# Optimization experiments

Measured on AMD Instinct MI355X. Metric: run time of the kernel, lower is better.

The kernel has to match this reference:

```python
import jax, jax.numpy as jnp
import numpy as np

EPS_R2 = 1e-12
EPS_POS = 1e-08
EPS_SUM = 1e-12


def _gaussian_psf(k, sigma):
    ax = np.arange(-k // 2 + 1.0, k // 2 + 1.0)
    xx, yy = np.meshgrid(ax, ax)
    g = np.exp(-(xx ** 2 + yy ** 2) / (2.0 * sigma ** 2))
    g = g / g.sum()
    return jnp.asarray(g.astype(np.float32))[None, None]  # (1,1,k,k)


def setup_inputs() -> dict:
    key = jax.random.key(0)
    k1, k2, k3 = jax.random.split(key, 3)
    B, C, H, W = 16, 1, 1024, 1024
    src = jax.random.normal(k1, (B, C, H, W), dtype=jnp.float32)
    raw_psf = _gaussian_psf(21, 3.0) + 0.001 * jax.random.normal(k2, (1, 1, 21, 21), dtype=jnp.float32)
    sub = 0.1 * jax.random.normal(k3, (2,), dtype=jnp.float32)
    return {
        "src": src,
        "raw_psf": raw_psf,
        "x0": jnp.float32(0.0),
        "y0": jnp.float32(0.0),
        "raw_b": jnp.float32(0.08),
        "raw_rc": jnp.float32(0.01),
        "raw_subpix": sub,
    }


def _bilinear_sample(src, gx, gy):
    # src: (B,C,H,W); gx, gy: (B,Hg,Wg) normalized coords in [-1,1],
    # align_corners=True, zeros padding (matches F.grid_sample).
    B, C, H, W = src.shape
    ix = (gx + 1.0) * 0.5 * (W - 1)
    iy = (gy + 1.0) * 0.5 * (H - 1)
    ix0 = jnp.floor(ix)
    iy0 = jnp.floor(iy)
    wx1 = ix - ix0
    wy1 = iy - iy0
    ix0i = ix0.astype(jnp.int32)
    iy0i = iy0.astype(jnp.int32)
    ix1i = ix0i + 1
    iy1i = iy0i + 1
    bidx = jnp.arange(B)[:, None, None]

    def corner(yi, xi, w):
        valid = (yi >= 0) & (yi < H) & (xi >= 0) & (xi < W)
        yc = jnp.clip(yi, 0, H - 1)
        xc = jnp.clip(xi, 0, W - 1)
        v = src[bidx, :, yc, xc]  # (B,Hg,Wg,C)
        return v * (w * valid)[..., None]

    out = (corner(iy0i, ix0i, (1.0 - wy1) * (1.0 - wx1))
           + corner(iy0i, ix1i, (1.0 - wy1) * wx1)
           + corner(iy1i, ix0i, wy1 * (1.0 - wx1))
           + corner(iy1i, ix1i, wy1 * wx1))
    return jnp.transpose(out, (0, 3, 1, 2))  # (B,C,Hg,Wg)


def reference(src, raw_psf, x0, y0, raw_b, raw_rc, raw_subpix):
    B, C, H, W = src.shape
    k = raw_psf.shape[-1]
    b = jax.nn.softplus(raw_b) + EPS_POS
    rc = jax.nn.softplus(raw_rc) + EPS_POS
    sub = 0.25 * jnp.tanh(raw_subpix)

    xs = jnp.linspace(-1.0, 1.0, W)
    ys = jnp.linspace(-1.0, 1.0, H)
    # torch.meshgrid(ys, xs, indexing='xy') semantics: shape (W, H),
    # yv[i,j] = ys[j], xv[i,j] = xs[i] (note: transposed vs usual HxW).
    yv, xv = jnp.meshgrid(ys, xs, indexing='xy')

    dx = xv - x0
    dy = yv - y0
    denom = jnp.sqrt(dx * dx + dy * dy + EPS_R2 + rc * rc)
    ax = b * dx / denom
    ay = b * dy / denom

    gx = jnp.broadcast_to(xv - ax + sub[0], (B, W, H))
    gy = jnp.broadcast_to(yv - ay + sub[1], (B, W, H))

    y_warp = _bilinear_sample(src, gx, gy)  # (B,C,W,H)

    psf = jnp.maximum(raw_psf, 0.0)
    psf = psf / jnp.maximum(psf.sum(axis=(2, 3), keepdims=True), EPS_SUM)
    pad = k // 2
    y_conv = jax.lax.conv_general_dilated(
        y_warp, psf, window_strides=(1, 1),
        padding=((pad, pad), (pad, pad)),
        dimension_numbers=("NCHW", "OIHW", "NCHW"))
    return y_conv
```

## Files before the change

### kernel.cpp

```cpp
#include <hip/hip_runtime.h>
#include <math.h>

#define WW 1024
#define HH 1024
#define TI 64
#define TJ 128
#define HALO_J 148
#define VALID_I 84
#define FILL_I 96
#define PITCH_T 104
#define AOFF 448
#define AOFF2 21952
#define YOFF 43520
#define NEED_WS (174080u + 33554432u)

typedef short short8 __attribute__((ext_vector_type(8)));
typedef float float16 __attribute__((ext_vector_type(16)));

__device__ __forceinline__ unsigned short f2bf(float f) {
    union { float f; unsigned int u; } c; c.f = f;
    unsigned int u = c.u;
    return (unsigned short)((u + 0x7FFFu + ((u >> 16) & 1u)) >> 16);
}

__device__ __forceinline__ float warp_sample(const float* __restrict__ sb, int I, int J,
                                             float bpar, float rc2, float sub0, float sub1,
                                             float x0, float y0) {
    const float SSTEP = 2.0f / 1023.0f;
    float yv = fmaf((float)J, SSTEP, -1.0f);
    float xv = fmaf((float)I, SSTEP, -1.0f);
    float dx = xv - x0;
    float dy = yv - y0;
    float s = bpar * __builtin_amdgcn_rsqf(dx * dx + dy * dy + rc2);
    float gx = xv - dx * s + sub0;
    float gy = yv - dy * s + sub1;
    float ix = (gx + 1.0f) * (0.5f * 1023.0f);
    float iy = (gy + 1.0f) * (0.5f * 1023.0f);
    float fx = floorf(ix), fy = floorf(iy);
    float wx1 = ix - fx, wy1 = iy - fy;
    float wx0 = 1.f - wx1, wy0 = 1.f - wy1;
    int xi0 = (int)fx, yi0 = (int)fy;
    int xi1 = xi0 + 1, yi1 = yi0 + 1;
    int xc0 = min(max(xi0, 0), WW - 1);
    int xc1 = min(max(xi1, 0), WW - 1);
    int yc0 = min(max(yi0, 0), HH - 1);
    int yc1 = min(max(yi1, 0), HH - 1);
    bool vx0 = (unsigned)xi0 < WW, vx1 = (unsigned)xi1 < WW;
    bool vy0 = (unsigned)yi0 < HH, vy1 = (unsigned)yi1 < HH;
    float w00 = (vx0 && vy0) ? wy0 * wx0 : 0.f;
    float w01 = (vx1 && vy0) ? wy0 * wx1 : 0.f;
    float w10 = (vx0 && vy1) ? wy1 * wx0 : 0.f;
    float w11 = (vx1 && vy1) ? wy1 * wx1 : 0.f;
    float v00 = sb[yc0 * WW + xc0];
    float v01 = sb[yc0 * WW + xc1];
    float v10 = sb[yc1 * WW + xc0];
    float v11 = sb[yc1 * WW + xc1];
    return v00 * w00 + v01 * w01 + v10 * w10 + v11 * w11;
}

__global__ void prep_kernel(const float* __restrict__ raw_psf,
                            const float* __restrict__ x0p, const float* __restrict__ y0p,
                            const float* __restrict__ raw_b, const float* __restrict__ raw_rc,
                            const float* __restrict__ raw_sub,
                            float* __restrict__ ws) {
    __shared__ float red[512];
    __shared__ float psn[441];
    int t = threadIdx.x;
    float v = 0.f;
    if (t < 441) v = fmaxf(raw_psf[t], 0.f);
    red[t] = v;
    __syncthreads();
    for (int s = 256; s > 0; s >>= 1) {
        if (t < s) red[t] += red[t + s];
        __syncthreads();
    }
    float sum = fmaxf(red[0], 1e-12f);
    if (t < 441) { float pn = v / sum; ws[t] = pn; psn[t] = pn; }
    if (t == 0) {
        float b  = log1pf(expf(raw_b[0]))  + 1e-8f;
        float rc = log1pf(expf(raw_rc[0])) + 1e-8f;
        ws[441] = b;
        ws[442] = 1e-12f + rc * rc;
        ws[443] = 0.25f * tanhf(raw_sub[0]);
        ws[444] = 0.25f * tanhf(raw_sub[1]);
        ws[445] = x0p[0];
        ws[446] = y0p[0];
    }
    __syncthreads();

    short* A  = (short*)(ws + AOFF);
    short* A2 = (short*)(ws + AOFF2);
    for (int g = t; g < 21 * 256; g += 512) {
        int vv = g >> 8;
        int r  = g & 255;
        int d  = r >> 6;
        int l  = r & 63;
        int m  = l & 31;
        int k0 = (l >> 5) << 3;
        short8 o8, o8b;
#pragma unroll
        for (int q = 0; q < 8; ++q) {
            int u = 16 * d + k0 + q - m;
            unsigned short pv = 0, pv2 = 0;
            if ((unsigned)u <= 20u) pv = f2bf(psn[u * 21 + vv]);
            int u2 = u - 6;
            if ((unsigned)u2 <= 20u) pv2 = f2bf(psn[u2 * 21 + vv]);
            o8[q]  = (short)pv;
            o8b[q] = (short)pv2;
        }
        *(short8*)&A[(size_t)g * 8]  = o8;
        *(short8*)&A2[(size_t)g * 8] = o8b;
    }
}

__global__ __launch_bounds__(256, 4) void warp_kernel(
        const float* __restrict__ src, const float* __restrict__ pp,
        unsigned short* __restrict__ yw) {
    const float bpar = pp[441], rc2 = pp[442];
    const float sub0 = pp[443], sub1 = pp[444];
    const float x0 = pp[445], y0 = pp[446];
    const int base = blockIdx.x * 8192;
    const int tid = threadIdx.x;
#pragma unroll 4
    for (int it = 0; it < 32; ++it) {
        int n = base + it * 256 + tid;
        int b0 = n >> 20;
        int J = (n >> 10) & 1023;
        int I = n & 1023;
        const float* sb = src + ((size_t)b0 << 20);
        float val = warp_sample(sb, I, J, bpar, rc2, sub0, sub1, x0, y0);
        yw[n] = f2bf(val);
    }
}

__global__ __launch_bounds__(256, 4) void conv_kernel(
        const unsigned short* __restrict__ yw, const float* __restrict__ pp,
        float* __restrict__ out) {
    __shared__ unsigned short ThT[HALO_J * PITCH_T];

    const int tid = threadIdx.x;
    const int j0 = blockIdx.x * TJ;
    const int i0 = blockIdx.y * TI;
    const int b0 = blockIdx.z;

    const unsigned short* wb = yw + ((size_t)b0 << 20);

    for (int p = tid; p < HALO_J * 12; p += 256) {
        int hc = (int)((unsigned)p / 12u);
        int c  = p - hc * 12;
        int J  = j0 - 10 + hc;
        int xs = i0 - 16 + c * 8;
        short8 d8 = {0, 0, 0, 0, 0, 0, 0, 0};
        if ((unsigned)J < HH && (unsigned)xs < WW)
            d8 = *(const short8*)&wb[J * WW + xs];
        *(short8*)&ThT[hc * PITCH_T + c * 8] = d8;
    }
    __syncthreads();

    const int lane = tid & 63;
    const int wv = tid >> 6;
    const int nrow = lane & 31;
    const int khalf = lane >> 5;

    float16 acc[2];
#pragma unroll
    for (int m = 0; m < 2; ++m)
#pragma unroll
        for (int q = 0; q < 16; ++q) acc[m][q] = 0.f;

    const short8* Aall = (const short8*)(pp + AOFF2);

#pragma unroll 1
    for (int v = 0; v < 21; ++v) {
        short8 Af[4];
#pragma unroll
        for (int d = 0; d < 4; ++d)
            Af[d] = Aall[(v * 4 + d) * 64 + lane];

        const unsigned short* bp = &ThT[(32 * wv + nrow + v) * PITCH_T + khalf * 8];
        short8 Bf[6];
#pragma unroll
        for (int c = 0; c < 6; ++c)
            Bf[c] = *(const short8*)&bp[16 * c];

#pragma unroll
        for (int mq = 0; mq < 2; ++mq) {
#pragma unroll
            for (int d = 0; d < 4; ++d)
                acc[mq] = __builtin_amdgcn_mfma_f32_32x32x16_bf16(
                    Af[d], Bf[2 * mq + d], acc[mq], 0, 0, 0);
        }
    }

    float* ob = out + (size_t)b0 * (WW * (size_t)HH);
    const int gj = j0 + 32 * wv + nrow;
#pragma unroll
    for (int mq = 0; mq < 2; ++mq) {
#pragma unroll
        for (int reg = 0; reg < 16; ++reg) {
            int row = (reg & 3) + 8 * (reg >> 2) + 4 * khalf;
            int gi = i0 + 32 * mq + row;
            ob[(size_t)gi * HH + gj] = acc[mq][reg];
        }
    }
}

__global__ __launch_bounds__(256, 4) void fused_kernel(
        const float* __restrict__ src, const float* __restrict__ pp,
        float* __restrict__ out) {
    __shared__ unsigned short ThT[HALO_J * PITCH_T];

    const int tid = threadIdx.x;
    const int j0 = blockIdx.x * TJ;
    const int i0 = blockIdx.y * TI;
    const int b0 = blockIdx.z;

    const float bpar = pp[441], rc2 = pp[442];
    const float sub0 = pp[443], sub1 = pp[444];
    const float x0 = pp[445], y0 = pp[446];

    const float* sb = src + (size_t)b0 * (HH * (size_t)WW);

    const int NELEM = HALO_J * FILL_I;
#pragma unroll 1
    for (int base = 0; base < NELEM; base += 1024) {
        float vals[4];
        int offs[4];
#pragma unroll
        for (int e = 0; e < 4; ++e) {
            int n = base + (e << 8) + tid;
            float val = 0.f;
            int off = -1;
            if (n < NELEM) {
                int hc = (int)((unsigned)n / 96u);
                int hr = n - hc * 96;
                off = hc * PITCH_T + hr;
                int J = j0 - 10 + hc;
                int I = i0 - 10 + hr;
                if (hr < VALID_I && (unsigned)J < HH && (unsigned)I < WW)
                    val = warp_sample(sb, I, J, bpar, rc2, sub0, sub1, x0, y0);
            }
            vals[e] = val;
            offs[e] = off;
        }
#pragma unroll
        for (int e = 0; e < 4; ++e) {
            if (offs[e] >= 0) ThT[offs[e]] = f2bf(vals[e]);
        }
    }
    __syncthreads();

    const int lane = tid & 63;
    const int wv = tid >> 6;
    const int nrow = lane & 31;
    const int khalf = lane >> 5;

    float16 acc[2];
#pragma unroll
    for (int m = 0; m < 2; ++m)
#pragma unroll
        for (int q = 0; q < 16; ++q) acc[m][q] = 0.f;

    const short8* Aall = (const short8*)(pp + AOFF);

#pragma unroll 1
    for (int v = 0; v < 21; ++v) {
        short8 Af[4];
#pragma unroll
        for (int d = 0; d < 4; ++d)
            Af[d] = Aall[(v * 4 + d) * 64 + lane];

        const unsigned short* bp = &ThT[(32 * wv + nrow + v) * PITCH_T + khalf * 8];
        short8 Bf[6];
#pragma unroll
        for (int c = 0; c < 6; ++c)
            Bf[c] = *(const short8*)&bp[16 * c];

#pragma unroll
        for (int mq = 0; mq < 2; ++mq) {
#pragma unroll
            for (int d = 0; d < 4; ++d)
                acc[mq] = __builtin_amdgcn_mfma_f32_32x32x16_bf16(
                    Af[d], Bf[2 * mq + d], acc[mq], 0, 0, 0);
        }
    }

    float* ob = out + (size_t)b0 * (WW * (size_t)HH);
    const int gj = j0 + 32 * wv + nrow;
#pragma unroll
    for (int mq = 0; mq < 2; ++mq) {
#pragma unroll
        for (int reg = 0; reg < 16; ++reg) {
            int row = (reg & 3) + 8 * (reg >> 2) + 4 * khalf;
            int gi = i0 + 32 * mq + row;
            ob[(size_t)gi * HH + gj] = acc[mq][reg];
        }
    }
}

extern "C" void kernel_launch(void* const* d_in, const int* in_sizes, int n_in,
                              void* d_out, int out_size, void* d_ws, size_t ws_size,
                              hipStream_t stream) {
    const float* src     = (const float*)d_in[0];
    const float* raw_psf = (const float*)d_in[1];
    const float* x0      = (const float*)d_in[2];
    const float* y0      = (const float*)d_in[3];
    const float* raw_b   = (const float*)d_in[4];
    const float* raw_rc  = (const float*)d_in[5];
    const float* raw_sub = (const float*)d_in[6];
    float* ws = (float*)d_ws;

    prep_kernel<<<1, 512, 0, stream>>>(raw_psf, x0, y0, raw_b, raw_rc, raw_sub, ws);

    dim3 grid(HH / TJ, WW / TI, 16);
    if (ws_size >= (size_t)NEED_WS) {
        unsigned short* yw = (unsigned short*)(ws + YOFF);
        warp_kernel<<<2048, 256, 0, stream>>>(src, ws, yw);
        conv_kernel<<<grid, 256, 0, stream>>>(yw, ws, (float*)d_out);
    } else {
        fused_kernel<<<grid, 256, 0, stream>>>(src, ws, (float*)d_out);
    }
}
```

Before: 216.9 us.

## Add in-bounds bilinear fast path in warp kernel and prefetch conv weights

Restructures the warp kernel so each block handles eight rows of one image and hoists per-row terms. It computes coordinates with a fast reciprocal square root and, when every lane of a wavefront is in bounds, does a plain 4-tap bilinear load without bounds checks; otherwise it falls back to the original sampler. The conv kernel now software-prefetches the next iteration's PSF fragments from global memory, hiding load latency behind the MFMAs. Risks are small numerical differences from rsq, and the prefetch reads one fragment past the last tap (v=21), which may step outside the weight array.

```diff
diff --git a/kernel.cpp b/kernel.cpp
--- a/kernel.cpp
+++ b/kernel.cpp
@@ -119,17 +119,68 @@
     const float bpar = pp[441], rc2 = pp[442];
     const float sub0 = pp[443], sub1 = pp[444];
     const float x0 = pp[445], y0 = pp[446];
-    const int base = blockIdx.x * 8192;
+    const float SSTEP = 2.0f / 1023.0f;
+
     const int tid = threadIdx.x;
-#pragma unroll 4
-    for (int it = 0; it < 32; ++it) {
-        int n = base + it * 256 + tid;
-        int b0 = n >> 20;
-        int J = (n >> 10) & 1023;
-        int I = n & 1023;
-        const float* sb = src + ((size_t)b0 << 20);
-        float val = warp_sample(sb, I, J, bpar, rc2, sub0, sub1, x0, y0);
-        yw[n] = f2bf(val);
+    const int nb  = blockIdx.x;
+    const int b0  = nb >> 7;
+    const int J0  = (nb & 127) << 3;
+    const float* sb = src + ((size_t)b0 << 20);
+    unsigned short* yb = yw + ((size_t)b0 << 20) + ((size_t)J0 << 10);
+
+#pragma unroll 1
+    for (int jr = 0; jr < 8; ++jr) {
+        int J = J0 + jr;
+        float yv = fmaf((float)J, SSTEP, -1.0f);
+        float dy = yv - y0;
+        float dyt = fmaf(dy, dy, rc2);
+        unsigned short* yrow = yb + (jr << 10);
+
+        float ixa[4], iya[4];
+        bool bad = false;
+#pragma unroll
+        for (int q = 0; q < 4; ++q) {
+            int I = (q << 8) + tid;
+            float xv = fmaf((float)I, SSTEP, -1.0f);
+            float dx = xv - x0;
+            float s  = bpar * __builtin_amdgcn_rsqf(fmaf(dx, dx, dyt));
+            float gx = xv - dx * s + sub0;
+            float gy = yv - dy * s + sub1;
+            ixa[q] = (gx + 1.0f) * (0.5f * 1023.0f);
+            iya[q] = (gy + 1.0f) * (0.5f * 1023.0f);
+            bad |= !(ixa[q] >= 0.f && ixa[q] < 1023.f &&
+                     iya[q] >= 0.f && iya[q] < 1023.f);
+        }
+        if (!__any(bad)) {
+            float v00[4], v01[4], v10[4], v11[4], fxs[4], fys[4];
+#pragma unroll
+            for (int q = 0; q < 4; ++q) {
+                float fx = floorf(ixa[q]), fy = floorf(iya[q]);
+                fxs[q] = fx; fys[q] = fy;
+                const float* p = sb + (((int)fy) << 10) + (int)fx;
+                v00[q] = p[0];
+                v01[q] = p[1];
+                v10[q] = p[WW];
+                v11[q] = p[WW + 1];
+            }
+#pragma unroll
+            for (int q = 0; q < 4; ++q) {
+                float wx1 = ixa[q] - fxs[q];
+                float wy1 = iya[q] - fys[q];
+                float wx0 = 1.f - wx1;
+                float r0 = fmaf(wx1, v01[q], wx0 * v00[q]);
+                float r1 = fmaf(wx1, v11[q], wx0 * v10[q]);
+                float val = fmaf(wy1, r1, (1.f - wy1) * r0);
+                yrow[(q << 8) + tid] = f2bf(val);
+            }
+        } else {
+#pragma unroll
+            for (int q = 0; q < 4; ++q) {
+                int I = (q << 8) + tid;
+                float val = warp_sample(sb, I, J, bpar, rc2, sub0, sub1, x0, y0);
+                yrow[(q << 8) + tid] = f2bf(val);
+            }
+        }
     }
 }
 
@@ -168,14 +219,19 @@
 #pragma unroll
         for (int q = 0; q < 16; ++q) acc[m][q] = 0.f;
 
-    const short8* Aall = (const short8*)(pp + AOFF2);
+    const short8* Ap = ((const short8*)(pp + AOFF2)) + lane;
+    short8 AfN[4];
+#pragma unroll
+    for (int d = 0; d < 4; ++d)
+        AfN[d] = Ap[d * 64];
 
 #pragma unroll 1
     for (int v = 0; v < 21; ++v) {
         short8 Af[4];
 #pragma unroll
-        for (int d = 0; d < 4; ++d)
-            Af[d] = Aall[(v * 4 + d) * 64 + lane];
+        for (int d = 0; d < 4; ++d) Af[d] = AfN[d];
+#pragma unroll
+        for (int d = 0; d < 4; ++d) AfN[d] = Ap[(v + 1) * 256 + d * 64];
 
         const unsigned short* bp = &ThT[(32 * wv + nrow + v) * PITCH_T + khalf * 8];
         short8 Bf[6];
```

After: 210.4 us. 1.03x faster.
